# Kernel tuning notes

Measured on AMD Instinct MI355X. Metric: run time of the kernel, lower is better.

The kernel has to match this reference:

```python
import jax, jax.numpy as jnp
import numpy as np

N_ATOMS = 4096
HSIZE = 128
N_HEADS = 8
D_K = HSIZE // N_HEADS


def setup_inputs() -> dict:
    key = jax.random.key(0)
    ks = jax.random.split(key, 11)
    s = 1.0 / np.sqrt(HSIZE)
    return {
        "query": jax.random.normal(ks[0], (N_ATOMS, HSIZE), dtype=jnp.float32),
        "key": jax.random.normal(ks[1], (N_ATOMS, HSIZE), dtype=jnp.float32),
        "value": jax.random.normal(ks[2], (N_ATOMS, HSIZE), dtype=jnp.float32),
        "mask": jax.random.randint(ks[3], (N_ATOMS, N_ATOMS), 0, 2, dtype=jnp.int32),
        "Wq": jax.random.normal(ks[4], (HSIZE, HSIZE), dtype=jnp.float32) * s,
        "bq": jnp.zeros((HSIZE,), dtype=jnp.float32),
        "Wk": jax.random.normal(ks[5], (HSIZE, HSIZE), dtype=jnp.float32) * s,
        "bk": jnp.zeros((HSIZE,), dtype=jnp.float32),
        "Wv": jax.random.normal(ks[6], (HSIZE, HSIZE), dtype=jnp.float32) * s,
        "bv": jnp.zeros((HSIZE,), dtype=jnp.float32),
        "Wo": jax.random.normal(ks[7], (HSIZE, HSIZE), dtype=jnp.float32) * s,
    }


def _mha(query, key, value, mask, Wq, bq, Wk, bk, Wv, bv, Wo):
    n = query.shape[0]
    # project and split heads: [n, hsize] -> [H, n, d_k]
    def heads(x, W, b):
        return (x @ W.T + b).reshape(n, N_HEADS, D_K).transpose(1, 0, 2)
    q = heads(query, Wq, bq)
    k = heads(key, Wk, bk)
    v = heads(value, Wv, bv)
    scale = 1.0 / jnp.sqrt(jnp.asarray(D_K, q.dtype))
    scores = jnp.einsum("hnd,hmd->hnm", q, k) * scale  # [H, n, n]
    scores = jnp.where(mask[None, :, :] == 0, jnp.asarray(-1e9, scores.dtype), scores)
    p_attn = jax.nn.softmax(scores, axis=-1)
    x = jnp.einsum("hnm,hmd->hnd", p_attn, v)  # [H, n, d_k]
    x = x.transpose(1, 0, 2).reshape(n, HSIZE)  # merge heads
    return x @ Wo.T  # output_linear has bias=False


def reference(query, key, value, mask, Wq, bq, Wk, bk, Wv, bv, Wo):
    return _mha(query, key, value, mask, Wq, bq, Wk, bk, Wv, bv, Wo)
```

## Files before the change

### kernel.cpp

```cpp
#include <hip/hip_runtime.h>
#include <hip/hip_bf16.h>

#define NA 4096
#define HS 128
#define PSTR 72
#define CSTR 136
#define MW 17

typedef unsigned short u16;
typedef unsigned long long u64;
using bf16x8  = __attribute__((ext_vector_type(8))) short;
using f32x4   = __attribute__((ext_vector_type(4))) float;
using ushort8 = __attribute__((ext_vector_type(8))) unsigned short;

#define QSCALE 0.18033688011112042f

static __device__ __forceinline__ u16 f2bf(float f) {
    unsigned u = __builtin_bit_cast(unsigned, f);
    u += 0x7FFFu + ((u >> 16) & 1u);
    return (u16)(u >> 16);
}

static __device__ __forceinline__ unsigned pkbf(float a, float b) {
    __hip_bfloat162 p = __float22bfloat162_rn(make_float2(a, b));
    unsigned r;
    __builtin_memcpy(&r, &p, 4);
    return r;
}

__global__ __launch_bounds__(256) void cvt_w(
    const float* __restrict__ Wq, const float* __restrict__ Wk,
    const float* __restrict__ Wv, const float* __restrict__ Wo,
    const float* __restrict__ bq, const float* __restrict__ bk,
    const float* __restrict__ bv,
    u16* __restrict__ Wf, float* __restrict__ bb)
{
    const int gid = blockIdx.x * 256 + threadIdx.x;
    const int e = gid * 4;
    const int mat = e >> 14, off = e & 16383;
    const float* src = (mat == 0) ? Wq : (mat == 1) ? Wk : (mat == 2) ? Wv : Wo;
    const float s = (mat == 0) ? QSCALE : 1.0f;
    float4 v = *(const float4*)(src + off);
    ushort4 o;
    o.x = f2bf(v.x * s); o.y = f2bf(v.y * s);
    o.z = f2bf(v.z * s); o.w = f2bf(v.w * s);
    const int j = off >> 7, k0 = off & 127;
    const int j0 = j >> 4, c = j & 15, kk = k0 >> 5, q = (k0 >> 3) & 3;
    const int tgt = mat * 16384 + ((j0 * 4 + kk) * 16 + c) * 32 + q * 8 + (k0 & 7);
    *(ushort4*)(Wf + tgt) = o;
    if (gid < 128)      bb[gid] = bq[gid] * QSCALE;
    else if (gid < 256) bb[gid] = bk[gid - 128];
    else if (gid < 384) bb[gid] = bv[gid - 256];
}

__global__ __launch_bounds__(256) void proj_mfma(
    const float* __restrict__ Xq, const float* __restrict__ Xk, const float* __restrict__ Xv,
    const u16* __restrict__ Wf, const float* __restrict__ bb,
    u16* __restrict__ Qbh, u16* __restrict__ Kbh, u16* __restrict__ VtB)
{
    const int mat = blockIdx.y;
    const float* X = (mat == 0) ? Xq : (mat == 1) ? Xk : Xv;
    const u16* Wm = Wf + mat * 16384;
    const float* bm = bb + mat * 128;
    const int r0b = blockIdx.x * 32;

    __shared__ __align__(16) u16 Xs[32 * CSTR];
    __shared__ __align__(16) u16 Cs[32 * CSTR];

    const int t = threadIdx.x;
    {
        const int r = t >> 3, cb = (t & 7) * 16;
        const float* Xr = X + (size_t)(r0b + r) * HS + cb;
#pragma unroll
        for (int seg = 0; seg < 4; ++seg) {
            float4 f = *(const float4*)(Xr + seg * 4);
            ushort4 u;
            u.x = f2bf(f.x); u.y = f2bf(f.y); u.z = f2bf(f.z); u.w = f2bf(f.w);
            *(ushort4*)(Xs + r * CSTR + cb + seg * 4) = u;
        }
    }
    __syncthreads();

    const int wv = t >> 6, lane = t & 63;
    const int c = lane & 15, q = lane >> 4;
    const int rw = (wv & 1) * 16;
    const int j0b = (wv >> 1) * 4;

    bf16x8 af[4];
#pragma unroll
    for (int kk = 0; kk < 4; ++kk)
        af[kk] = *(const bf16x8*)(Xs + (rw + c) * CSTR + kk * 32 + q * 8);

    const f32x4 zero = {0.f, 0.f, 0.f, 0.f};
#pragma unroll
    for (int jj = 0; jj < 4; ++jj) {
        const int j0 = j0b + jj;
        f32x4 acc = zero;
#pragma unroll
        for (int kk = 0; kk < 4; ++kk) {
            bf16x8 bf = *(const bf16x8*)(Wm + (j0 * 4 + kk) * 512 + c * 32 + q * 8);
            acc = __builtin_amdgcn_mfma_f32_16x16x32_bf16(af[kk], bf, acc, 0, 0, 0);
        }
        const float bias = bm[j0 * 16 + c];
#pragma unroll
        for (int r = 0; r < 4; ++r)
            Cs[(rw + 4 * q + r) * CSTR + j0 * 16 + c] = f2bf(acc[r] + bias);
    }
    __syncthreads();

    if (mat < 2) {
        u16* dst = (mat == 0) ? Qbh : Kbh;
        const int h8 = t >> 5, r = t & 31;
        const u16* src = Cs + r * CSTR + h8 * 16;
        u16* dp = dst + (size_t)h8 * (NA * 16) + (size_t)(r0b + r) * 16;
        *(bf16x8*)(dp)     = *(const bf16x8*)(src);
        *(bf16x8*)(dp + 8) = *(const bf16x8*)(src + 8);
    } else {
        const int d = t >> 1, s = t & 1;
        const int kb = r0b >> 6, ko = (r0b & 32) + s * 16;
        ushort8 v0, v1;
#pragma unroll
        for (int jj = 0; jj < 8; ++jj) v0[jj] = Cs[(s * 16 + jj) * CSTR + d];
#pragma unroll
        for (int jj = 0; jj < 8; ++jj) v1[jj] = Cs[(s * 16 + 8 + jj) * CSTR + d];
        u16* dp = VtB + (size_t)kb * 8192 + d * 64 + ko;
        *(ushort8*)(dp)     = v0;
        *(ushort8*)(dp + 8) = v1;
    }
}

__global__ __launch_bounds__(512, 6) void attn(
    const int* __restrict__ mask,
    const u16* __restrict__ Qbh, const u16* __restrict__ Kbh, const u16* __restrict__ VtB,
    float* __restrict__ part)
{
    __shared__ __align__(16) u16 Pbuf[8 * 16 * PSTR];
    __shared__ __align__(8)  u64 Mwp[16 * MW];

    const int t = threadIdx.x;
    const int h = t >> 6;
    const int lane = t & 63;
    const int c = lane & 15;
    const int q = lane >> 4;
    const int tile = blockIdx.x, split = blockIdx.y;
    const int i0 = tile * 16;
    const int kt0 = split * 1024;

#pragma unroll 4
    for (int rr = 0; rr < 32; ++rr) {
        const int idx = h * 32 + rr;
        const int row = idx >> 4, wc = idx & 15;
        const int v = mask[(size_t)(i0 + row) * NA + kt0 + wc * 64 + lane];
        u64 b = __ballot(v != 0);
        if (lane == 0) Mwp[row * MW + wc] = b;
    }

    const u16* Qh = Qbh + (size_t)h * (NA * 16);
    const u16* Kh = Kbh + (size_t)h * (NA * 16);
    const bf16x8 qf = *(const bf16x8*)(Qh + (size_t)(i0 + c) * 16 + (q & 1) * 8);

    __syncthreads();

    const f32x4 zero = {0.f, 0.f, 0.f, 0.f};
    f32x4 Oacc = zero;
    float lsum = 0.f;
    volatile u16* Pw = Pbuf + h * 16 * PSTR;

#pragma unroll 2
    for (int it = 0; it < 16; ++it) {
        const int kt = kt0 + it * 64;

        f32x4 ST[4];
#pragma unroll
        for (int t4 = 0; t4 < 4; ++t4) {
            bf16x8 kf = *(const bf16x8*)(Kh + (size_t)(kt + t4 * 16 + c) * 16 + (q & 1) * 8);
            ST[t4] = __builtin_amdgcn_mfma_f32_16x16x32_bf16(kf, qf, zero, 0, 0, 0);
        }
        const u16* Vb = VtB + (size_t)(kt >> 6) * 8192 + (h * 16 + c) * 64;
        bf16x8 vf0 = *(const bf16x8*)(Vb + q * 8);
        bf16x8 vf1 = *(const bf16x8*)(Vb + 32 + q * 8);

        u64 w = Mwp[c * MW + it] >> (4 * q);
        const unsigned mlo = (unsigned)w, mhi = (unsigned)(w >> 32);

#pragma unroll
        for (int t4 = 0; t4 < 4; ++t4) {
            const unsigned mw = (t4 < 2) ? mlo : mhi;
            const int sh = (t4 & 1) * 16;
            float p0 = ((mw >> (sh + 0)) & 1) ? __builtin_amdgcn_exp2f(ST[t4][0]) : 0.f;
            float p1 = ((mw >> (sh + 1)) & 1) ? __builtin_amdgcn_exp2f(ST[t4][1]) : 0.f;
            float p2 = ((mw >> (sh + 2)) & 1) ? __builtin_amdgcn_exp2f(ST[t4][2]) : 0.f;
            float p3 = ((mw >> (sh + 3)) & 1) ? __builtin_amdgcn_exp2f(ST[t4][3]) : 0.f;
            lsum += (p0 + p1) + (p2 + p3);
            const unsigned lo = pkbf(p0, p1);
            const unsigned hi = pkbf(p2, p3);
            *(volatile u64*)(Pw + c * PSTR + t4 * 16 + 4 * q) =
                (u64)lo | ((u64)hi << 32);
        }
        __builtin_amdgcn_s_waitcnt(0xC07F);

        bf16x8 pf0 = *(volatile const bf16x8*)(Pw + c * PSTR + q * 8);
        bf16x8 pf1 = *(volatile const bf16x8*)(Pw + c * PSTR + 32 + q * 8);
        Oacc = __builtin_amdgcn_mfma_f32_16x16x32_bf16(pf0, vf0, Oacc, 0, 0, 0);
        Oacc = __builtin_amdgcn_mfma_f32_16x16x32_bf16(pf1, vf1, Oacc, 0, 0, 0);
    }

    lsum += __shfl_xor(lsum, 16, 64);
    lsum += __shfl_xor(lsum, 32, 64);

    float* base = part + (size_t)((tile * 4 + split) * 8 + h) * 272;
#pragma unroll
    for (int r = 0; r < 4; ++r)
        base[(4 * q + r) * 16 + c] = Oacc[r];
    if (q == 0) base[256 + c] = lsum;
}

__global__ __launch_bounds__(256) void reduce_out(
    const float* __restrict__ part, const u16* __restrict__ Wf,
    float* __restrict__ out)
{
    __shared__ __align__(16) u16 xs[16 * CSTR];

    const int t = threadIdx.x;
    const int tile = blockIdx.x;
    const int i0 = tile * 16;
    const float* Pt = part + (size_t)tile * 4 * 8 * 272;

    {
        const int i = t >> 4, d = t & 15;
#pragma unroll
        for (int h = 0; h < 8; ++h) {
            float os = 0.f, ls = 0.f;
#pragma unroll
            for (int s = 0; s < 4; ++s) {
                const float* b = Pt + (size_t)(s * 8 + h) * 272;
                os += b[i * 16 + d];
                ls += b[256 + i];
            }
            xs[i * CSTR + h * 16 + d] = f2bf(os / ls);
        }
    }
    __syncthreads();

    const int wv = t >> 6, lane = t & 63;
    const int c = lane & 15, q = lane >> 4;
    const u16* WoB = Wf + 3 * 16384;

    bf16x8 af[4];
#pragma unroll
    for (int kk = 0; kk < 4; ++kk)
        af[kk] = *(const bf16x8*)(xs + c * CSTR + kk * 32 + q * 8);

    const f32x4 zero = {0.f, 0.f, 0.f, 0.f};
#pragma unroll
    for (int jj = 0; jj < 2; ++jj) {
        const int j0 = wv * 2 + jj;
        f32x4 acc = zero;
#pragma unroll
        for (int kk = 0; kk < 4; ++kk) {
            bf16x8 bf = *(const bf16x8*)(WoB + (j0 * 4 + kk) * 512 + c * 32 + q * 8);
            acc = __builtin_amdgcn_mfma_f32_16x16x32_bf16(af[kk], bf, acc, 0, 0, 0);
        }
#pragma unroll
        for (int r = 0; r < 4; ++r)
            out[(size_t)(i0 + 4 * q + r) * HS + j0 * 16 + c] = acc[r];
    }
}

extern "C" void kernel_launch(void* const* d_in, const int* in_sizes, int n_in,
                              void* d_out, int out_size, void* d_ws, size_t ws_size,
                              hipStream_t stream) {
    const float* query = (const float*)d_in[0];
    const float* key   = (const float*)d_in[1];
    const float* value = (const float*)d_in[2];
    const int*   mask  = (const int*)d_in[3];
    const float* Wq    = (const float*)d_in[4];
    const float* bq    = (const float*)d_in[5];
    const float* Wk    = (const float*)d_in[6];
    const float* bk    = (const float*)d_in[7];
    const float* Wv    = (const float*)d_in[8];
    const float* bv    = (const float*)d_in[9];
    const float* Wo    = (const float*)d_in[10];

    u16* Qbh = (u16*)d_ws;
    u16* Kbh = Qbh + (size_t)NA * HS;
    u16* VtB = Kbh + (size_t)NA * HS;
    u16* Wf  = VtB + (size_t)NA * HS;
    float* bb    = (float*)(Wf + 4 * 16384);
    float* partb = bb + 384;

    cvt_w<<<64, 256, 0, stream>>>(Wq, Wk, Wv, Wo, bq, bk, bv, Wf, bb);
    proj_mfma<<<dim3(128, 3), 256, 0, stream>>>(query, key, value, Wf, bb, Qbh, Kbh, VtB);
    attn<<<dim3(256, 4), 512, 0, stream>>>(mask, Qbh, Kbh, VtB, partb);
    reduce_out<<<256, 256, 0, stream>>>(partb, Wf, (float*)d_out);
}
```

Before: 193.7 us.

## Keep softmax probabilities in registers by permuting V layout to match MFMA fragments

The attention kernel no longer writes bf16 probabilities to LDS and reads them back for the P·V MFMA. Instead, the V-transpose writer in the projection kernel permutes the key ordering so that each lane's own packed probabilities line up with the MFMA A-operand layout. This removes the LDS round trip and its wait from the inner loop, and frees the shared Pbuf. The launch-bounds occupancy hint is also dropped, which could change register allocation.

```diff
diff --git a/kernel.cpp b/kernel.cpp
--- a/kernel.cpp
+++ b/kernel.cpp
@@ -3,7 +3,6 @@
 
 #define NA 4096
 #define HS 128
-#define PSTR 72
 #define CSTR 136
 #define MW 17
 
@@ -11,6 +10,7 @@
 typedef unsigned long long u64;
 using bf16x8  = __attribute__((ext_vector_type(8))) short;
 using f32x4   = __attribute__((ext_vector_type(4))) float;
+using u32x4   = __attribute__((ext_vector_type(4))) unsigned int;
 using ushort8 = __attribute__((ext_vector_type(8))) unsigned short;
 
 #define QSCALE 0.18033688011112042f
@@ -117,25 +117,28 @@
         *(bf16x8*)(dp + 8) = *(const bf16x8*)(src + 8);
     } else {
         const int d = t >> 1, s = t & 1;
-        const int kb = r0b >> 6, ko = (r0b & 32) + s * 16;
-        ushort8 v0, v1;
-#pragma unroll
-        for (int jj = 0; jj < 8; ++jj) v0[jj] = Cs[(s * 16 + jj) * CSTR + d];
-#pragma unroll
-        for (int jj = 0; jj < 8; ++jj) v1[jj] = Cs[(s * 16 + 8 + jj) * CSTR + d];
-        u16* dp = VtB + (size_t)kb * 8192 + d * 64 + ko;
-        *(ushort8*)(dp)     = v0;
-        *(ushort8*)(dp + 8) = v1;
-    }
-}
-
-__global__ __launch_bounds__(512, 6) void attn(
+        const int kb = r0b >> 6;
+        const int t4 = ((r0b & 32) >> 4) + s;
+        const int sec = t4 >> 1, half = t4 & 1;
+        u16* dp = VtB + (size_t)kb * 8192 + d * 64 + sec * 32 + half * 4;
+#pragma unroll
+        for (int qd = 0; qd < 4; ++qd) {
+            ushort4 vv;
+            vv.x = Cs[(s * 16 + qd * 4 + 0) * CSTR + d];
+            vv.y = Cs[(s * 16 + qd * 4 + 1) * CSTR + d];
+            vv.z = Cs[(s * 16 + qd * 4 + 2) * CSTR + d];
+            vv.w = Cs[(s * 16 + qd * 4 + 3) * CSTR + d];
+            *(ushort4*)(dp + qd * 8) = vv;
+        }
+    }
+}
+
+__global__ __launch_bounds__(512) void attn(
     const int* __restrict__ mask,
     const u16* __restrict__ Qbh, const u16* __restrict__ Kbh, const u16* __restrict__ VtB,
     float* __restrict__ part)
 {
-    __shared__ __align__(16) u16 Pbuf[8 * 16 * PSTR];
-    __shared__ __align__(8)  u64 Mwp[16 * MW];
+    __shared__ __align__(8) u64 Mwp[16 * MW];
 
     const int t = threadIdx.x;
     const int h = t >> 6;
@@ -164,25 +167,27 @@
     const f32x4 zero = {0.f, 0.f, 0.f, 0.f};
     f32x4 Oacc = zero;
     float lsum = 0.f;
-    volatile u16* Pw = Pbuf + h * 16 * PSTR;
 
 #pragma unroll 2
     for (int it = 0; it < 16; ++it) {
         const int kt = kt0 + it * 64;
 
+        const u16* Kp = Kh + (size_t)(kt + c) * 16 + (q & 1) * 8;
         f32x4 ST[4];
 #pragma unroll
         for (int t4 = 0; t4 < 4; ++t4) {
-            bf16x8 kf = *(const bf16x8*)(Kh + (size_t)(kt + t4 * 16 + c) * 16 + (q & 1) * 8);
+            bf16x8 kf = *(const bf16x8*)(Kp + t4 * 256);
             ST[t4] = __builtin_amdgcn_mfma_f32_16x16x32_bf16(kf, qf, zero, 0, 0, 0);
         }
-        const u16* Vb = VtB + (size_t)(kt >> 6) * 8192 + (h * 16 + c) * 64;
-        bf16x8 vf0 = *(const bf16x8*)(Vb + q * 8);
-        bf16x8 vf1 = *(const bf16x8*)(Vb + 32 + q * 8);
+
+        const u16* Vb = VtB + (size_t)(kt >> 6) * 8192 + (h * 16 + c) * 64 + q * 8;
+        bf16x8 vf0 = *(const bf16x8*)(Vb);
+        bf16x8 vf1 = *(const bf16x8*)(Vb + 32);
 
         u64 w = Mwp[c * MW + it] >> (4 * q);
         const unsigned mlo = (unsigned)w, mhi = (unsigned)(w >> 32);
 
+        unsigned pk[4][2];
 #pragma unroll
         for (int t4 = 0; t4 < 4; ++t4) {
             const unsigned mw = (t4 < 2) ? mlo : mhi;
@@ -192,17 +197,15 @@
             float p2 = ((mw >> (sh + 2)) & 1) ? __builtin_amdgcn_exp2f(ST[t4][2]) : 0.f;
             float p3 = ((mw >> (sh + 3)) & 1) ? __builtin_amdgcn_exp2f(ST[t4][3]) : 0.f;
             lsum += (p0 + p1) + (p2 + p3);
-            const unsigned lo = pkbf(p0, p1);
-            const unsigned hi = pkbf(p2, p3);
-            *(volatile u64*)(Pw + c * PSTR + t4 * 16 + 4 * q) =
-                (u64)lo | ((u64)hi << 32);
-        }
-        __builtin_amdgcn_s_waitcnt(0xC07F);
-
-        bf16x8 pf0 = *(volatile const bf16x8*)(Pw + c * PSTR + q * 8);
-        bf16x8 pf1 = *(volatile const bf16x8*)(Pw + c * PSTR + 32 + q * 8);
-        Oacc = __builtin_amdgcn_mfma_f32_16x16x32_bf16(pf0, vf0, Oacc, 0, 0, 0);
-        Oacc = __builtin_amdgcn_mfma_f32_16x16x32_bf16(pf1, vf1, Oacc, 0, 0, 0);
+            pk[t4][0] = pkbf(p0, p1);
+            pk[t4][1] = pkbf(p2, p3);
+        }
+        u32x4 a0 = {pk[0][0], pk[0][1], pk[1][0], pk[1][1]};
+        u32x4 a1 = {pk[2][0], pk[2][1], pk[3][0], pk[3][1]};
+        Oacc = __builtin_amdgcn_mfma_f32_16x16x32_bf16(
+            __builtin_bit_cast(bf16x8, a0), vf0, Oacc, 0, 0, 0);
+        Oacc = __builtin_amdgcn_mfma_f32_16x16x32_bf16(
+            __builtin_bit_cast(bf16x8, a1), vf1, Oacc, 0, 0, 0);
     }
 
     lsum += __shfl_xor(lsum, 16, 64);
```

Result: slower. 199.0 us (+2.7%).
